# Kernel optimization log

Measured on AMD Instinct MI355X. Metric: run time of the kernel, lower is better.

The kernel has to match this reference:

```python
import jax, jax.numpy as jnp
import numpy as np

F0, F1 = 10, 10  # num_neighbor_list fanouts
B = 4096         # sampled pos+neg edges


def setup_inputs() -> dict:
    key = jax.random.key(0)
    ks = jax.random.split(key, 24)
    def rn(k, shp, scale=0.05):
        return (jax.random.normal(k, shp, dtype=jnp.float32) * scale)
    inp = {
        "user_feat": rn(ks[0], (50000, 512), 1.0),
        "item_feat": rn(ks[1], (100000, 512), 1.0),
        "W_pu": rn(ks[2], (512, 256)), "b_pu": jnp.zeros((256,), jnp.float32),
        "W_pi": rn(ks[3], (512, 256)), "b_pi": jnp.zeros((256,), jnp.float32),
        "u_self0": rn(ks[4], (256, 256)), "u_agg0": rn(ks[5], (256, 256)),
        "u_self1": rn(ks[6], (256, 128)), "u_agg1": rn(ks[7], (256, 128)),
        "i_self0": rn(ks[8], (256, 256)), "i_agg0": rn(ks[9], (256, 256)),
        "i_self1": rn(ks[10], (256, 128)), "i_agg1": rn(ks[11], (256, 128)),
        "W_lin": rn(ks[12], (128, 1)), "b_lin": jnp.zeros((1,), jnp.float32),
        # precomputed multi-hop sampled node ids (alternating user/item spaces)
        "src_h0": jax.random.randint(ks[13], (B,), 0, 50000, dtype=jnp.int32),
        "src_h1": jax.random.randint(ks[14], (B * F0,), 0, 100000, dtype=jnp.int32),
        "src_h2": jax.random.randint(ks[15], (B * F0 * F1,), 0, 50000, dtype=jnp.int32),
        "dst_h0": jax.random.randint(ks[16], (B,), 0, 100000, dtype=jnp.int32),
        "dst_h1": jax.random.randint(ks[17], (B * F0,), 0, 50000, dtype=jnp.int32),
        "dst_h2": jax.random.randint(ks[18], (B * F0 * F1,), 0, 100000, dtype=jnp.int32),
    }
    return inp


def _sage(h0, h1, h2, Wself0, Wagg0, Wself1, Wagg1):
    # 2-layer GraphSAGE with mean aggregation over fixed fanouts.
    d = h0.shape[-1]
    # layer 0: update hop-0 and hop-1 representations
    n0 = h1.reshape(h0.shape[0], F0, d).mean(axis=1)          # [B, d]
    g0 = jax.nn.relu(h0 @ Wself0 + n0 @ Wagg0)                # [B, H0]
    n1 = h2.reshape(h1.shape[0], F1, d).mean(axis=1)          # [B*F0, d]
    g1 = jax.nn.relu(h1 @ Wself0 + n1 @ Wagg0)                # [B*F0, H0]
    # layer 1: final hop-0 representation (no activation on last layer)
    n = g1.reshape(g0.shape[0], F0, -1).mean(axis=1)          # [B, H0]
    return g0 @ Wself1 + n @ Wagg1                            # [B, H1]


def reference(user_feat, item_feat, W_pu, b_pu, W_pi, b_pi,
              u_self0, u_agg0, u_self1, u_agg1,
              i_self0, i_agg0, i_self1, i_agg1,
              W_lin, b_lin,
              src_h0, src_h1, src_h2, dst_h0, dst_h1, dst_h2):
    u_proj = jax.nn.sigmoid(user_feat @ W_pu + b_pu)   # [U, P]
    i_proj = jax.nn.sigmoid(item_feat @ W_pi + b_pi)   # [I, P]
    # src side alternates user/item per hop; dst side alternates item/user
    user_h = _sage(u_proj[src_h0], i_proj[src_h1], u_proj[src_h2],
                   u_self0, u_agg0, u_self1, u_agg1)
    item_h = _sage(i_proj[dst_h0], u_proj[dst_h1], i_proj[dst_h2],
                   i_self0, i_agg0, i_self1, i_agg1)
    logits = (user_h * item_h) @ W_lin + b_lin          # [B, 1]
    return logits
```

## Files before the change

kernel.cpp:

```cpp
#include <hip/hip_runtime.h>
#include <hip/hip_bf16.h>
#include <type_traits>

typedef __attribute__((ext_vector_type(8))) short short8;
typedef __attribute__((ext_vector_type(4))) float f32x4;
typedef unsigned short u16;
typedef unsigned int u32;

typedef const __attribute__((address_space(1))) u32* gp1_t;
typedef __attribute__((address_space(3))) u32* lp3_t;

__device__ __forceinline__ float bf2f(u16 u) {
    union { unsigned int i; float f; } x; x.i = ((unsigned int)u) << 16; return x.f;
}
__device__ __forceinline__ u16 f2bf(float f) {
    union { __hip_bfloat16 h; u16 u; } c; c.h = __float2bfloat16(f); return c.u;
}
__device__ __forceinline__ short8 cvt8(float4 v0, float4 v1) {
    union { u16 u[8]; short8 s; } p;
    p.u[0] = f2bf(v0.x); p.u[1] = f2bf(v0.y); p.u[2] = f2bf(v0.z); p.u[3] = f2bf(v0.w);
    p.u[4] = f2bf(v1.x); p.u[5] = f2bf(v1.y); p.u[6] = f2bf(v1.z); p.u[7] = f2bf(v1.w);
    return p.s;
}
__device__ __forceinline__ void gload_lds16(const void* g, void* l) {
    __builtin_amdgcn_global_load_lds((gp1_t)g, (lp3_t)l, 16, 0, 0);
}

struct TCJobs {
    const float* A[6];
    const float* Bm[6];
    u16* out[6];
    int N[6];
    int Ka[6];
};

__global__ void transcat6_k(TCJobs j) {
    int jid = blockIdx.y;
    int i = blockIdx.x * 256 + threadIdx.x;
    int N = j.N[jid];
    if (i >= N * 512) return;
    int n = i >> 9, k = i & 511, Ka = j.Ka[jid];
    float v = (k < Ka) ? j.A[jid][k * N + n] : j.Bm[jid][(k - Ka) * N + n];
    j.out[jid][i] = f2bf(v);
}

struct GJob {
    const void* A;
    const u16* WT;
    const float* bias;
    void* C;
    int M;
    int nct;
    int toff;
};
struct GJobs4 { GJob j[4]; };

template <int NJ, bool F32A, int ACT, bool OF32>
__global__ __launch_bounds__(256, 4) void gemm_k(GJobs4 js) {
    const int K = 512;
    __shared__ __align__(1024) char As[16384];
    __shared__ __align__(1024) char Bs[16384];
    const int t = threadIdx.x;
    const int lane = t & 63;
    const int wid = t >> 6;
    const int wr = wid >> 1, wc = wid & 1;
    const int lr = lane & 15;

    const int nwg = gridDim.x, p = blockIdx.x;
    const int q = nwg >> 3, rr = nwg & 7;
    const int xcd = p & 7, idx = p >> 3;
    const int L = (xcd < rr ? xcd * (q + 1) : rr * (q + 1) + (xcd - rr) * q) + idx;

    GJob jb = js.j[0];
    #pragma unroll
    for (int k = 1; k < NJ; ++k) if (L >= js.j[k].toff) jb = js.j[k];
    const int tl = L - jb.toff;
    const int rt = (jb.nct == 2) ? (tl >> 1) : tl;
    const int ct = (jb.nct == 2) ? (tl & 1) : 0;
    const int row_base = rt * 128, col_base = ct * 128;
    const int M = jb.M, N = jb.nct << 7;

    f32x4 acc[4][4] = {};

    for (int kt = 0; kt < K; kt += 64) {
        #pragma unroll
        for (int i = 0; i < 4; ++i) {
            int slot = wid * 4 + i;
            int rl = slot * 8 + (lane >> 3);
            int sc = (lane & 7) ^ (rl & 7);
            gload_lds16(&jb.WT[(size_t)(col_base + rl) * K + kt + sc * 8], &Bs[slot * 1024]);
        }
        if constexpr (F32A) {
            const float* Af = (const float*)jb.A;
            #pragma unroll
            for (int i = 0; i < 4; ++i) {
                int c = i * 256 + t;
                int row = c >> 3, cc = c & 7;
                int gr = row_base + row; if (gr >= M) gr = M - 1;
                const float* src = &Af[(size_t)gr * K + kt + cc * 8];
                float4 v0 = *(const float4*)src;
                float4 v1 = *(const float4*)(src + 4);
                *(short8*)&As[(row * 128 + cc * 16) ^ ((row & 7) << 4)] = cvt8(v0, v1);
            }
        } else {
            const u16* Ab = (const u16*)jb.A;
            #pragma unroll
            for (int i = 0; i < 4; ++i) {
                int slot = wid * 4 + i;
                int rl = slot * 8 + (lane >> 3);
                int sc = (lane & 7) ^ (rl & 7);
                int gr = row_base + rl; if (gr >= M) gr = M - 1;
                gload_lds16(&Ab[(size_t)gr * K + kt + sc * 8], &As[slot * 1024]);
            }
        }
        __syncthreads();

        #pragma unroll
        for (int ks = 0; ks < 2; ++ks) {
            const int g = ks * 4 + (lane >> 4);
            short8 a[4], b[4];
            #pragma unroll
            for (int ni = 0; ni < 4; ++ni) {
                int r = wc * 64 + ni * 16 + lr;
                b[ni] = *(const short8*)&Bs[(r * 128 + g * 16) ^ ((r & 7) << 4)];
            }
            #pragma unroll
            for (int mi = 0; mi < 4; ++mi) {
                int r = wr * 64 + mi * 16 + lr;
                a[mi] = *(const short8*)&As[(r * 128 + g * 16) ^ ((r & 7) << 4)];
            }
            #pragma unroll
            for (int mi = 0; mi < 4; ++mi)
                #pragma unroll
                for (int ni = 0; ni < 4; ++ni)
                    acc[mi][ni] = __builtin_amdgcn_mfma_f32_16x16x32_bf16(
                        a[mi], b[ni], acc[mi][ni], 0, 0, 0);
        }
        __syncthreads();
    }

    #pragma unroll
    for (int mi = 0; mi < 4; ++mi) {
        int row0 = row_base + wr * 64 + mi * 16 + ((lane >> 4) << 2);
        #pragma unroll
        for (int ni = 0; ni < 4; ++ni) {
            int col = col_base + wc * 64 + ni * 16 + lr;
            float bv = jb.bias ? jb.bias[col] : 0.f;
            #pragma unroll
            for (int r = 0; r < 4; ++r) {
                int row = row0 + r;
                if (row < M) {
                    float x = acc[mi][ni][r] + bv;
                    if (ACT == 1) x = fmaxf(x, 0.f);
                    if (ACT == 2) x = 1.f / (1.f + __expf(-x));
                    if constexpr (OF32)
                        ((float*)jb.C)[(size_t)row * N + col] = x;
                    else
                        ((u16*)jb.C)[(size_t)row * N + col] = f2bf(x);
                }
            }
        }
    }
}

struct BJob {
    u16* X;
    const u16* selfP;
    const int* sidx;
    const u16* nbP;
    const int* nidx;
    int roff;
};
struct BJobs4 { BJob j[4]; };

template <int NJ>
__global__ void build_xm_k(BJobs4 bj, int total) {
    int gw = (int)((blockIdx.x * blockDim.x + threadIdx.x) >> 5);
    int hl = threadIdx.x & 31;
    if (gw >= total) return;
    BJob jb = bj.j[0];
    #pragma unroll
    for (int k = 1; k < NJ; ++k) if (gw >= bj.j[k].roff) jb = bj.j[k];
    int r = gw - jb.roff;

    int c8 = hl * 8;
    int sr = jb.sidx ? jb.sidx[r] : r;
    short8 sv = *(const short8*)&jb.selfP[(size_t)sr * 256 + c8];
    *(short8*)&jb.X[(size_t)r * 512 + c8] = sv;

    float s[8] = {};
    #pragma unroll
    for (int f = 0; f < 10; ++f) {
        int nr = jb.nidx ? jb.nidx[r * 10 + f] : r * 10 + f;
        short8 nv = *(const short8*)&jb.nbP[(size_t)nr * 256 + c8];
        #pragma unroll
        for (int jj = 0; jj < 8; ++jj) s[jj] += bf2f((u16)nv[jj]);
    }
    union { u16 u[8]; short8 v; } o;
    #pragma unroll
    for (int jj = 0; jj < 8; ++jj) o.u[jj] = f2bf(s[jj] * 0.1f);
    *(short8*)&jb.X[(size_t)r * 512 + 256 + c8] = o.v;
}

__global__ void logits_k(const float* __restrict__ hu, const float* __restrict__ hi,
                         const float* __restrict__ wlin, const float* __restrict__ blin,
                         float* __restrict__ out, int Bn) {
    int w = (blockIdx.x * blockDim.x + threadIdx.x) >> 6;
    int lane = threadIdx.x & 63;
    if (w >= Bn) return;
    float s = 0.f;
    #pragma unroll
    for (int k = lane; k < 128; k += 64)
        s += hu[(size_t)w * 128 + k] * hi[(size_t)w * 128 + k] * wlin[k];
    #pragma unroll
    for (int off = 32; off > 0; off >>= 1) s += __shfl_down(s, off, 64);
    if (lane == 0) out[w] = s + blin[0];
}

extern "C" void kernel_launch(void* const* d_in, const int* in_sizes, int n_in,
                              void* d_out, int out_size, void* d_ws, size_t ws_size,
                              hipStream_t stream) {
    const float* user_feat = (const float*)d_in[0];
    const float* item_feat = (const float*)d_in[1];
    const float* W_pu = (const float*)d_in[2];
    const float* b_pu = (const float*)d_in[3];
    const float* W_pi = (const float*)d_in[4];
    const float* b_pi = (const float*)d_in[5];
    const float* u_self0 = (const float*)d_in[6];
    const float* u_agg0 = (const float*)d_in[7];
    const float* u_self1 = (const float*)d_in[8];
    const float* u_agg1 = (const float*)d_in[9];
    const float* i_self0 = (const float*)d_in[10];
    const float* i_agg0 = (const float*)d_in[11];
    const float* i_self1 = (const float*)d_in[12];
    const float* i_agg1 = (const float*)d_in[13];
    const float* W_lin = (const float*)d_in[14];
    const float* b_lin = (const float*)d_in[15];
    const int* src_h0 = (const int*)d_in[16];
    const int* src_h1 = (const int*)d_in[17];
    const int* src_h2 = (const int*)d_in[18];
    const int* dst_h0 = (const int*)d_in[19];
    const int* dst_h1 = (const int*)d_in[20];
    const int* dst_h2 = (const int*)d_in[21];
    float* out = (float*)d_out;

    const int NU = 50000, NI = 100000, B = 4096, BF = 40960;

    char* ws = (char*)d_ws;
    size_t off = 0;
    auto alloc = [&](size_t bytes) -> void* {
        void* p = ws + off;
        off += (bytes + 255) & ~(size_t)255;
        return p;
    };
    u16* Pu   = (u16*)alloc((size_t)NU * 256 * 2);
    u16* Pi   = (u16*)alloc((size_t)NI * 256 * 2);
    u16* X1a  = (u16*)alloc((size_t)BF * 512 * 2);
    u16* X1b  = (u16*)alloc((size_t)BF * 512 * 2);
    u16* G1a  = (u16*)alloc((size_t)BF * 256 * 2);
    u16* G1b  = (u16*)alloc((size_t)BF * 256 * 2);
    u16* X0a  = (u16*)alloc((size_t)B * 512 * 2);
    u16* X0b  = (u16*)alloc((size_t)B * 512 * 2);
    u16* G0a  = (u16*)alloc((size_t)B * 256 * 2);
    u16* G0b  = (u16*)alloc((size_t)B * 256 * 2);
    u16* X2a  = (u16*)alloc((size_t)B * 512 * 2);
    u16* X2b  = (u16*)alloc((size_t)B * 512 * 2);
    float* Hu = (float*)alloc((size_t)B * 128 * 4);
    float* Hi = (float*)alloc((size_t)B * 128 * 4);
    u16* WpuT = (u16*)alloc(256 * 512 * 2);
    u16* WpiT = (u16*)alloc(256 * 512 * 2);
    u16* W0uT = (u16*)alloc(256 * 512 * 2);
    u16* W0iT = (u16*)alloc(256 * 512 * 2);
    u16* W1uT = (u16*)alloc(128 * 512 * 2);
    u16* W1iT = (u16*)alloc(128 * 512 * 2);

    TCJobs tj;
    tj.A[0] = W_pu;    tj.Bm[0] = W_pu;    tj.out[0] = WpuT; tj.N[0] = 256; tj.Ka[0] = 512;
    tj.A[1] = W_pi;    tj.Bm[1] = W_pi;    tj.out[1] = WpiT; tj.N[1] = 256; tj.Ka[1] = 512;
    tj.A[2] = u_self0; tj.Bm[2] = u_agg0;  tj.out[2] = W0uT; tj.N[2] = 256; tj.Ka[2] = 256;
    tj.A[3] = i_self0; tj.Bm[3] = i_agg0;  tj.out[3] = W0iT; tj.N[3] = 256; tj.Ka[3] = 256;
    tj.A[4] = u_self1; tj.Bm[4] = u_agg1;  tj.out[4] = W1uT; tj.N[4] = 128; tj.Ka[4] = 256;
    tj.A[5] = i_self1; tj.Bm[5] = i_agg1;  tj.out[5] = W1iT; tj.N[5] = 128; tj.Ka[5] = 256;
    transcat6_k<<<dim3(512, 6), 256, 0, stream>>>(tj);

    const int ptu = ((NU + 127) / 128) * 2;
    const int pti = ((NI + 127) / 128) * 2;
    GJobs4 pj;
    pj.j[0] = {user_feat, WpuT, b_pu, Pu, NU, 2, 0};
    pj.j[1] = {item_feat, WpiT, b_pi, Pi, NI, 2, ptu};
    pj.j[2] = pj.j[1]; pj.j[3] = pj.j[1];
    gemm_k<2, true, 2, false><<<ptu + pti, 256, 0, stream>>>(pj);

    BJobs4 b1;
    b1.j[0] = {X1a, Pi, src_h1, Pu, src_h2, 0};
    b1.j[1] = {X1b, Pu, dst_h1, Pi, dst_h2, BF};
    b1.j[2] = {X0a, Pu, src_h0, Pi, src_h1, 2 * BF};
    b1.j[3] = {X0b, Pi, dst_h0, Pu, dst_h1, 2 * BF + B};
    const int tot1 = 2 * BF + 2 * B;
    build_xm_k<4><<<tot1 / 8, 256, 0, stream>>>(b1, tot1);

    GJobs4 sj;
    sj.j[0] = {X1a, W0uT, nullptr, G1a, BF, 2, 0};
    sj.j[1] = {X1b, W0iT, nullptr, G1b, BF, 2, 640};
    sj.j[2] = {X0a, W0uT, nullptr, G0a, B, 2, 1280};
    sj.j[3] = {X0b, W0iT, nullptr, G0b, B, 2, 1344};
    gemm_k<4, false, 1, false><<<1408, 256, 0, stream>>>(sj);

    BJobs4 b2;
    b2.j[0] = {X2a, G0a, nullptr, G1a, nullptr, 0};
    b2.j[1] = {X2b, G0b, nullptr, G1b, nullptr, B};
    b2.j[2] = b2.j[1]; b2.j[3] = b2.j[1];
    build_xm_k<2><<<(2 * B) / 8, 256, 0, stream>>>(b2, 2 * B);

    GJobs4 fj;
    fj.j[0] = {X2a, W1uT, nullptr, Hu, B, 1, 0};
    fj.j[1] = {X2b, W1iT, nullptr, Hi, B, 1, 32};
    fj.j[2] = fj.j[1]; fj.j[3] = fj.j[1];
    gemm_k<2, false, 0, true><<<64, 256, 0, stream>>>(fj);

    logits_k<<<B / 4, 256, 0, stream>>>(Hu, Hi, W_lin, b_lin, out, B);
}
```

Before: 309.5 us.

## Halve GEMM K-tile and load fp32 A directly to LDS, converting at fragment read

The GEMM K-step drops from 64 to 32, halving the bf16 LDS buffers and removing the XOR swizzle for bf16 tiles. The fp32 A operand is now copied straight into LDS with async global-to-LDS loads instead of being loaded into registers and converted before storing. The bf16 conversion moves to the fragment read from LDS. This aims to cut register staging and VGPR pressure and let the loads run asynchronously. In exchange there are twice as many barrier iterations, conversion work is repeated per wave, and the unswizzled bf16 reads may hit LDS bank conflicts.

```diff
diff --git a/kernel.cpp b/kernel.cpp
--- a/kernel.cpp
+++ b/kernel.cpp
@@ -58,8 +58,8 @@
 template <int NJ, bool F32A, int ACT, bool OF32>
 __global__ __launch_bounds__(256, 4) void gemm_k(GJobs4 js) {
     const int K = 512;
-    __shared__ __align__(1024) char As[16384];
-    __shared__ __align__(1024) char Bs[16384];
+    __shared__ __align__(1024) char As[F32A ? 16384 : 8192];
+    __shared__ __align__(1024) char Bs[8192];
     const int t = threadIdx.x;
     const int lane = t & 63;
     const int wid = t >> 6;
@@ -82,52 +82,55 @@
 
     f32x4 acc[4][4] = {};
 
-    for (int kt = 0; kt < K; kt += 64) {
+    for (int kt = 0; kt < K; kt += 32) {
         #pragma unroll
-        for (int i = 0; i < 4; ++i) {
-            int slot = wid * 4 + i;
-            int rl = slot * 8 + (lane >> 3);
-            int sc = (lane & 7) ^ (rl & 7);
-            gload_lds16(&jb.WT[(size_t)(col_base + rl) * K + kt + sc * 8], &Bs[slot * 1024]);
+        for (int i = 0; i < 2; ++i) {
+            int slot = wid * 2 + i;
+            int rl = slot * 16 + (lane >> 2);
+            int cc = lane & 3;
+            gload_lds16(&jb.WT[(size_t)(col_base + rl) * K + kt + cc * 8], &Bs[slot * 1024]);
         }
         if constexpr (F32A) {
-            const float* Af = (const float*)jb.A;
-            #pragma unroll
-            for (int i = 0; i < 4; ++i) {
-                int c = i * 256 + t;
-                int row = c >> 3, cc = c & 7;
-                int gr = row_base + row; if (gr >= M) gr = M - 1;
-                const float* src = &Af[(size_t)gr * K + kt + cc * 8];
-                float4 v0 = *(const float4*)src;
-                float4 v1 = *(const float4*)(src + 4);
-                *(short8*)&As[(row * 128 + cc * 16) ^ ((row & 7) << 4)] = cvt8(v0, v1);
-            }
-        } else {
-            const u16* Ab = (const u16*)jb.A;
             #pragma unroll
             for (int i = 0; i < 4; ++i) {
                 int slot = wid * 4 + i;
                 int rl = slot * 8 + (lane >> 3);
                 int sc = (lane & 7) ^ (rl & 7);
                 int gr = row_base + rl; if (gr >= M) gr = M - 1;
-                gload_lds16(&Ab[(size_t)gr * K + kt + sc * 8], &As[slot * 1024]);
+                gload_lds16(&((const float*)jb.A)[(size_t)gr * K + kt + sc * 4],
+                            &As[slot * 1024]);
+            }
+        } else {
+            #pragma unroll
+            for (int i = 0; i < 2; ++i) {
+                int slot = wid * 2 + i;
+                int rl = slot * 16 + (lane >> 2);
+                int cc = lane & 3;
+                int gr = row_base + rl; if (gr >= M) gr = M - 1;
+                gload_lds16(&((const u16*)jb.A)[(size_t)gr * K + kt + cc * 8],
+                            &As[slot * 1024]);
             }
         }
         __syncthreads();
 
-        #pragma unroll
-        for (int ks = 0; ks < 2; ++ks) {
-            const int g = ks * 4 + (lane >> 4);
+        {
+            const int g = lane >> 4;
             short8 a[4], b[4];
             #pragma unroll
             for (int ni = 0; ni < 4; ++ni) {
                 int r = wc * 64 + ni * 16 + lr;
-                b[ni] = *(const short8*)&Bs[(r * 128 + g * 16) ^ ((r & 7) << 4)];
+                b[ni] = *(const short8*)&Bs[r * 64 + g * 16];
             }
             #pragma unroll
             for (int mi = 0; mi < 4; ++mi) {
                 int r = wr * 64 + mi * 16 + lr;
-                a[mi] = *(const short8*)&As[(r * 128 + g * 16) ^ ((r & 7) << 4)];
+                if constexpr (F32A) {
+                    float4 v0 = *(const float4*)&As[r * 128 + ((2 * g) ^ (r & 7)) * 16];
+                    float4 v1 = *(const float4*)&As[r * 128 + ((2 * g + 1) ^ (r & 7)) * 16];
+                    a[mi] = cvt8(v0, v1);
+                } else {
+                    a[mi] = *(const short8*)&As[r * 64 + g * 16];
+                }
             }
             #pragma unroll
             for (int mi = 0; mi < 4; ++mi)
```

Measured after the change: 307.0 us. Within noise of the previous version (-0.8%).
